# Kernel tuning notes

Measured on AMD Instinct MI355X. Metric: run time of the kernel, lower is better.

## Reference

```python
import jax, jax.numpy as jnp
import numpy as np

HEADS = 8
WS = 16
EPS = 1e-6


def setup_inputs() -> dict:
    key = jax.random.key(0)
    k1, k2 = jax.random.split(key)
    x = jax.random.normal(k1, (4, 64, 512, 512), dtype=jnp.float32)
    w_qkv = jax.random.normal(k2, (192, 64), dtype=jnp.float32) * 0.05  # 1x1 conv: [3*dim, dim]
    return {"x": x, "w_qkv": w_qkv}


def _elu1(t):
    return jax.nn.elu(t) + 1.0


def _lwmsa(x, w_qkv):
    B, C, H, W = x.shape
    ws, h = WS, HEADS
    d = C // h
    ph, pw = (-H) % ws, (-W) % ws
    if ph or pw:
        x = jnp.pad(x, ((0, 0), (0, 0), (0, ph), (0, pw)))
    Hp, Wp = H + ph, W + pw
    hh, ww = Hp // ws, Wp // ws
    # 1x1 conv == channel matmul
    qkv = jnp.einsum('oc,bchw->bohw', w_qkv, x)  # [B, 3C, Hp, Wp]
    # 'b (qkv h d) (hh ws1) (ww ws2) -> qkv (b hh ww) h d (ws1 ws2)'
    qkv = qkv.reshape(B, 3, h, d, hh, ws, ww, ws)
    qkv = qkv.transpose(1, 0, 4, 6, 2, 3, 5, 7).reshape(3, B * hh * ww, h, d, ws * ws)
    q, k, v = qkv[0], qkv[1], qkv[2]  # each [Bw, h, d, n]

    feat = None  # carried across heads, [Bw, d, n]
    feats = []
    for i in range(h):
        qi, ki, vi = q[:, i], k[:, i], v[:, i]
        if i > 0:
            qi, ki, vi = qi + feat, ki + feat, vi + feat
        qf = _elu1(qi).transpose(0, 2, 1)   # [Bw, n, d]
        kf = _elu1(ki)                      # [Bw, d, n]
        ksum = jnp.sum(kf, axis=-1) + EPS   # [Bw, d]
        # original: einsum('bhnm,bhc->bhn', q, ksum) sums m and c INDEPENDENTLY
        z = 1.0 / (jnp.sum(qf, axis=-1) * jnp.sum(ksum, axis=-1, keepdims=True))  # [Bw, n]
        kv = jnp.einsum('bdn,bcn->bdc', kf, vi)          # [Bw, d, d]
        feat = jnp.einsum('bnd,bdc,bn->bcn', qf, kv, z)  # [Bw, d, n]
        feats.append(feat)

    out = jnp.stack(feats, axis=1)  # [Bw, h, d, n]
    # '(b hh ww) h d (ws1 ws2) -> b (h d) (hh ws1) (ww ws2)'
    out = out.reshape(B, hh, ww, h, d, ws, ws)
    out = out.transpose(0, 3, 4, 1, 5, 2, 6).reshape(B, C, Hp, Wp)
    return out[:, :, :H, :W]


def reference(x, w_qkv):
    return _lwmsa(x, w_qkv)
```

## Files before the change

kernel.cpp:

```cpp
#include <hip/hip_runtime.h>

#define HW (512 * 512)
#define QP 260
#define WN 12288

typedef __bf16 bf16;
typedef __attribute__((ext_vector_type(8))) __bf16 bf16x8;
typedef __attribute__((ext_vector_type(4))) float f32x4;

__device__ __forceinline__ void cvt_split(float f, bf16& h, bf16& l) {
    h = (bf16)f;
    l = (bf16)(f - (float)h);
}

__global__ __launch_bounds__(256) void wcvt_kernel(
    const float* __restrict__ w, bf16* __restrict__ wh, bf16* __restrict__ wl)
{
    const int i = blockIdx.x * 256 + threadIdx.x;
    if (i < WN) {
        bf16 h, l;
        cvt_split(w[i], h, l);
        wh[i] = h;
        wl[i] = l;
    }
}

__global__ __launch_bounds__(256, 2) void lwmsa_kernel(
    const float* __restrict__ x,
    const bf16* __restrict__ wh,
    const bf16* __restrict__ wl,
    float* __restrict__ out)
{
    const int win  = blockIdx.x;
    const int b    = win >> 10;
    const int wrow = (win >> 5) & 31;
    const int wcol = win & 31;
    const int n    = threadIdx.x;
    const int lane = n & 63;
    const int wvid = n >> 6;
    const int c16  = lane & 15;
    const int q4   = lane >> 4;

    const int base = b * (64 * HW) + (wrow * 16 + (n >> 4)) * 512 + wcol * 16 + (n & 15);
    const int xwin = b * (64 * HW) + (wrow * 16) * 512 + wcol * 16;

    __shared__ float qk[24 * QP];
    __shared__ float kvp[4 * 64];
    __shared__ float kv_s[64];
    __shared__ float tp[2][4];

    bf16x8 ah[2][4], al[2][4];
    #pragma unroll
    for (int ks = 0; ks < 2; ++ks)
        #pragma unroll
        for (int mt = 0; mt < 4; ++mt) {
            const int row = wvid * 4 + mt;
            const float* xp = x + xwin + row * 512 + c16 + (ks * 32 + q4 * 8) * HW;
            #pragma unroll
            for (int j = 0; j < 8; ++j) {
                bf16 h, l;
                cvt_split(xp[j * HW], h, l);
                ah[ks][mt][j] = h;
                al[ks][mt][j] = l;
            }
        }

    auto mfma_stage = [&](int hh) {
        f32x4 acc[4][2];
        #pragma unroll
        for (int mt = 0; mt < 4; ++mt)
            #pragma unroll
            for (int nt = 0; nt < 2; ++nt)
                acc[mt][nt] = (f32x4){0.f, 0.f, 0.f, 0.f};

        #pragma unroll
        for (int ks = 0; ks < 2; ++ks) {
            #pragma unroll
            for (int nt = 0; nt < 2; ++nt) {
                const int ml   = nt * 16 + c16;
                const int grow = (ml < 24) ? ((ml >> 3) * 64 + hh * 8 + (ml & 7))
                                           : (hh * 8);
                const int off  = grow * 64 + ks * 32 + q4 * 8;
                const bf16x8 bh = *(const bf16x8*)&wh[off];
                const bf16x8 bl = *(const bf16x8*)&wl[off];
                #pragma unroll
                for (int mt = 0; mt < 4; ++mt) {
                    acc[mt][nt] = __builtin_amdgcn_mfma_f32_16x16x32_bf16(ah[ks][mt], bh, acc[mt][nt], 0, 0, 0);
                    acc[mt][nt] = __builtin_amdgcn_mfma_f32_16x16x32_bf16(al[ks][mt], bh, acc[mt][nt], 0, 0, 0);
                    acc[mt][nt] = __builtin_amdgcn_mfma_f32_16x16x32_bf16(ah[ks][mt], bl, acc[mt][nt], 0, 0, 0);
                }
            }
        }

        #pragma unroll
        for (int nt = 0; nt < 2; ++nt) {
            const int ml = nt * 16 + c16;
            if (ml < 24) {
                #pragma unroll
                for (int mt = 0; mt < 4; ++mt) {
                    const int px = (wvid * 4 + mt) * 16 + q4 * 4;
                    *(float4*)&qk[ml * QP + px] = *(float4*)&acc[mt][nt];
                }
            }
        }
    };

    float feat[8];
    #pragma unroll
    for (int d = 0; d < 8; ++d) feat[d] = 0.f;

    mfma_stage(0);
    __syncthreads();

    for (int h = 0; h < 8; ++h) {
        float qf[8];
        float Sq = 0.f, tpart = 0.f;
        #pragma unroll
        for (int d = 0; d < 8; ++d) {
            const float aq = qk[d * QP + n]        + feat[d];
            const float ak = qk[(8 + d) * QP + n]  + feat[d];
            const float av = qk[(16 + d) * QP + n] + feat[d];
            qf[d] = aq > 0.f ? aq + 1.f : __expf(aq);
            const float kf = ak > 0.f ? ak + 1.f : __expf(ak);
            Sq    += qf[d];
            tpart += kf;
            qk[(8 + d) * QP + n]  = kf;
            qk[(16 + d) * QP + n] = av;
        }

        #pragma unroll
        for (int off = 1; off < 64; off <<= 1)
            tpart += __shfl_xor(tpart, off, 64);
        if (lane == 0) tp[h & 1][wvid] = tpart;

        asm volatile("s_waitcnt lgkmcnt(0)" ::: "memory");

        {
            const float4* kr = (const float4*)(qk + (8 + (lane >> 3)) * QP + wvid * 64);
            const float4* vr = (const float4*)(qk + (16 + (lane & 7)) * QP + wvid * 64);
            float s0 = 0.f, s1 = 0.f, s2 = 0.f, s3 = 0.f;
            #pragma unroll
            for (int j = 0; j < 16; ++j) {
                const float4 kk = kr[j];
                const float4 vv = vr[j];
                s0 = fmaf(kk.x, vv.x, s0);
                s1 = fmaf(kk.y, vv.y, s1);
                s2 = fmaf(kk.z, vv.z, s2);
                s3 = fmaf(kk.w, vv.w, s3);
            }
            kvp[wvid * 64 + lane] = (s0 + s1) + (s2 + s3);
        }

        __syncthreads();

        if (n < 64)
            kv_s[n] = (kvp[n] + kvp[64 + n]) + (kvp[128 + n] + kvp[192 + n]);

        if (h < 7)
            mfma_stage(h + 1);

        __syncthreads();

        const float T  = ((tp[h & 1][0] + tp[h & 1][1]) + (tp[h & 1][2] + tp[h & 1][3])) + 8.0f * 1e-6f;
        const float zi = 1.0f / (Sq * T);

        float ft[8];
        #pragma unroll
        for (int d = 0; d < 8; ++d) ft[d] = 0.f;
        #pragma unroll
        for (int d = 0; d < 8; ++d) {
            const float qd = qf[d];
            const float4 a  = ((const float4*)(kv_s + d * 8))[0];
            const float4 bb = ((const float4*)(kv_s + d * 8))[1];
            ft[0] = fmaf(qd, a.x,  ft[0]);
            ft[1] = fmaf(qd, a.y,  ft[1]);
            ft[2] = fmaf(qd, a.z,  ft[2]);
            ft[3] = fmaf(qd, a.w,  ft[3]);
            ft[4] = fmaf(qd, bb.x, ft[4]);
            ft[5] = fmaf(qd, bb.y, ft[5]);
            ft[6] = fmaf(qd, bb.z, ft[6]);
            ft[7] = fmaf(qd, bb.w, ft[7]);
        }
        #pragma unroll
        for (int d = 0; d < 8; ++d) {
            feat[d] = ft[d] * zi;
            out[base + (h * 8 + d) * HW] = feat[d];
        }
    }
}

extern "C" void kernel_launch(void* const* d_in, const int* in_sizes, int n_in,
                              void* d_out, int out_size, void* d_ws, size_t ws_size,
                              hipStream_t stream) {
    const float* x  = (const float*)d_in[0];
    const float* w  = (const float*)d_in[1];
    float* out      = (float*)d_out;
    bf16* wh = (bf16*)d_ws;
    bf16* wl = wh + WN;
    wcvt_kernel<<<dim3((WN + 255) / 256), dim3(256), 0, stream>>>(w, wh, wl);
    lwmsa_kernel<<<dim3(4096), dim3(256), 0, stream>>>(x, wh, wl, out);
}
```

Before: 279.5 us.

## Process two adjacent windows per block to amortize syncs and weight loads

Each block now handles two horizontally adjacent 16x16 windows instead of one, so the grid shrinks from 4096 to 2048 blocks. Shared buffers, register fragments and per-head state are duplicated per window, and both windows' MFMA stages and reductions share the same barriers and weight-fragment loads. The aim is to amortize barrier latency and per-block overhead and to give each wave more independent work between syncs. In exchange it doubles register and LDS use (qk alone becomes about 50KB), which may cut occupancy below the two-blocks-per-CU launch bound.

```diff
diff --git a/kernel.cpp b/kernel.cpp
--- a/kernel.cpp
+++ b/kernel.cpp
@@ -31,41 +31,49 @@
     const bf16* __restrict__ wl,
     float* __restrict__ out)
 {
-    const int win  = blockIdx.x;
-    const int b    = win >> 10;
-    const int wrow = (win >> 5) & 31;
-    const int wcol = win & 31;
+    const int blk  = blockIdx.x;
+    const int b    = blk >> 9;
+    const int wrow = (blk >> 4) & 31;
+    const int wp   = blk & 15;
     const int n    = threadIdx.x;
     const int lane = n & 63;
     const int wvid = n >> 6;
     const int c16  = lane & 15;
     const int q4   = lane >> 4;
 
-    const int base = b * (64 * HW) + (wrow * 16 + (n >> 4)) * 512 + wcol * 16 + (n & 15);
-    const int xwin = b * (64 * HW) + (wrow * 16) * 512 + wcol * 16;
-
-    __shared__ float qk[24 * QP];
-    __shared__ float kvp[4 * 64];
-    __shared__ float kv_s[64];
-    __shared__ float tp[2][4];
-
-    bf16x8 ah[2][4], al[2][4];
+    __shared__ float qk[2][24 * QP];
+    __shared__ float kvp[2][4 * 64];
+    __shared__ float kv_s[2][64];
+    __shared__ float tp[2][2][4];
+
+    int base[2], xwin[2];
     #pragma unroll
-    for (int ks = 0; ks < 2; ++ks)
-        #pragma unroll
-        for (int mt = 0; mt < 4; ++mt) {
-            const int row = wvid * 4 + mt;
-            const float* xp = x + xwin + row * 512 + c16 + (ks * 32 + q4 * 8) * HW;
-            #pragma unroll
-            for (int j = 0; j < 8; ++j) {
-                bf16 h, l;
-                cvt_split(xp[j * HW], h, l);
-                ah[ks][mt][j] = h;
-                al[ks][mt][j] = l;
-            }
-        }
-
-    auto mfma_stage = [&](int hh) {
+    for (int w = 0; w < 2; ++w) {
+        const int wcol = wp * 2 + w;
+        base[w] = b * (64 * HW) + (wrow * 16 + (n >> 4)) * 512 + wcol * 16 + (n & 15);
+        xwin[w] = b * (64 * HW) + (wrow * 16) * 512 + wcol * 16;
+    }
+
+    bf16x8 ah[2][2][4], al[2][2][4];
+    #pragma unroll
+    for (int w = 0; w < 2; ++w)
+        #pragma unroll
+        for (int ks = 0; ks < 2; ++ks)
+            #pragma unroll
+            for (int mt = 0; mt < 4; ++mt) {
+                const int row = wvid * 4 + mt;
+                const float* xp = x + xwin[w] + row * 512 + c16 + (ks * 32 + q4 * 8) * HW;
+                #pragma unroll
+                for (int j = 0; j < 8; ++j) {
+                    bf16 h, l;
+                    cvt_split(xp[j * HW], h, l);
+                    ah[w][ks][mt][j] = h;
+                    al[w][ks][mt][j] = l;
+                }
+            }
+
+    auto mfma_stage = [&](const bf16x8 (&Ah)[2][4], const bf16x8 (&Al)[2][4],
+                          float* __restrict__ qkb, int hh) {
         f32x4 acc[4][2];
         #pragma unroll
         for (int mt = 0; mt < 4; ++mt)
@@ -85,9 +93,9 @@
                 const bf16x8 bl = *(const bf16x8*)&wl[off];
                 #pragma unroll
                 for (int mt = 0; mt < 4; ++mt) {
-                    acc[mt][nt] = __builtin_amdgcn_mfma_f32_16x16x32_bf16(ah[ks][mt], bh, acc[mt][nt], 0, 0, 0);
-                    acc[mt][nt] = __builtin_amdgcn_mfma_f32_16x16x32_bf16(al[ks][mt], bh, acc[mt][nt], 0, 0, 0);
-                    acc[mt][nt] = __builtin_amdgcn_mfma_f32_16x16x32_bf16(ah[ks][mt], bl, acc[mt][nt], 0, 0, 0);
+                    acc[mt][nt] = __builtin_amdgcn_mfma_f32_16x16x32_bf16(Ah[ks][mt], bh, acc[mt][nt], 0, 0, 0);
+                    acc[mt][nt] = __builtin_amdgcn_mfma_f32_16x16x32_bf16(Al[ks][mt], bh, acc[mt][nt], 0, 0, 0);
+                    acc[mt][nt] = __builtin_amdgcn_mfma_f32_16x16x32_bf16(Ah[ks][mt], bl, acc[mt][nt], 0, 0, 0);
                 }
             }
         }
@@ -99,45 +107,57 @@
                 #pragma unroll
                 for (int mt = 0; mt < 4; ++mt) {
                     const int px = (wvid * 4 + mt) * 16 + q4 * 4;
-                    *(float4*)&qk[ml * QP + px] = *(float4*)&acc[mt][nt];
+                    *(float4*)&qkb[ml * QP + px] = *(float4*)&acc[mt][nt];
                 }
             }
         }
     };
 
-    float feat[8];
+    float feat[2][8];
     #pragma unroll
-    for (int d = 0; d < 8; ++d) feat[d] = 0.f;
-
-    mfma_stage(0);
+    for (int w = 0; w < 2; ++w)
+        #pragma unroll
+        for (int d = 0; d < 8; ++d) feat[w][d] = 0.f;
+
+    mfma_stage(ah[0], al[0], qk[0], 0);
+    mfma_stage(ah[1], al[1], qk[1], 0);
     __syncthreads();
 
     for (int h = 0; h < 8; ++h) {
-        float qf[8];
-        float Sq = 0.f, tpart = 0.f;
-        #pragma unroll
-        for (int d = 0; d < 8; ++d) {
-            const float aq = qk[d * QP + n]        + feat[d];
-            const float ak = qk[(8 + d) * QP + n]  + feat[d];
-            const float av = qk[(16 + d) * QP + n] + feat[d];
-            qf[d] = aq > 0.f ? aq + 1.f : __expf(aq);
-            const float kf = ak > 0.f ? ak + 1.f : __expf(ak);
-            Sq    += qf[d];
-            tpart += kf;
-            qk[(8 + d) * QP + n]  = kf;
-            qk[(16 + d) * QP + n] = av;
-        }
-
-        #pragma unroll
-        for (int off = 1; off < 64; off <<= 1)
-            tpart += __shfl_xor(tpart, off, 64);
-        if (lane == 0) tp[h & 1][wvid] = tpart;
+        float qf[2][8], Sq[2], tpart[2];
+        #pragma unroll
+        for (int w = 0; w < 2; ++w) {
+            Sq[w] = 0.f; tpart[w] = 0.f;
+            #pragma unroll
+            for (int d = 0; d < 8; ++d) {
+                const float aq = qk[w][d * QP + n]        + feat[w][d];
+                const float ak = qk[w][(8 + d) * QP + n]  + feat[w][d];
+                const float av = qk[w][(16 + d) * QP + n] + feat[w][d];
+                qf[w][d] = aq > 0.f ? aq + 1.f : __expf(aq);
+                const float kf = ak > 0.f ? ak + 1.f : __expf(ak);
+                Sq[w]    += qf[w][d];
+                tpart[w] += kf;
+                qk[w][(8 + d) * QP + n]  = kf;
+                qk[w][(16 + d) * QP + n] = av;
+            }
+        }
+
+        #pragma unroll
+        for (int off = 1; off < 64; off <<= 1) {
+            tpart[0] += __shfl_xor(tpart[0], off, 64);
+            tpart[1] += __shfl_xor(tpart[1], off, 64);
+        }
+        if (lane == 0) {
+            tp[0][h & 1][wvid] = tpart[0];
+            tp[1][h & 1][wvid] = tpart[1];
+        }
 
         asm volatile("s_waitcnt lgkmcnt(0)" ::: "memory");
 
-        {
-            const float4* kr = (const float4*)(qk + (8 + (lane >> 3)) * QP + wvid * 64);
-            const float4* vr = (const float4*)(qk + (16 + (lane & 7)) * QP + wvid * 64);
+        #pragma unroll
+        for (int w = 0; w < 2; ++w) {
+            const float4* kr = (const float4*)(qk[w] + (8 + (lane >> 3)) * QP + wvid * 64);
+            const float4* vr = (const float4*)(qk[w] + (16 + (lane & 7)) * QP + wvid * 64);
             float s0 = 0.f, s1 = 0.f, s2 = 0.f, s3 = 0.f;
             #pragma unroll
             for (int j = 0; j < 16; ++j) {
@@ -148,43 +168,53 @@
                 s2 = fmaf(kk.z, vv.z, s2);
                 s3 = fmaf(kk.w, vv.w, s3);
             }
-            kvp[wvid * 64 + lane] = (s0 + s1) + (s2 + s3);
+            kvp[w][wvid * 64 + lane] = (s0 + s1) + (s2 + s3);
         }
 
         __syncthreads();
 
-        if (n < 64)
-            kv_s[n] = (kvp[n] + kvp[64 + n]) + (kvp[128 + n] + kvp[192 + n]);
-
-        if (h < 7)
-            mfma_stage(h + 1);
+        if (n < 64) {
+            kv_s[0][n] = (kvp[0][n] + kvp[0][64 + n]) + (kvp[0][128 + n] + kvp[0][192 + n]);
+        } else if (n < 128) {
+            const int m = n - 64;
+            kv_s[1][m] = (kvp[1][m] + kvp[1][64 + m]) + (kvp[1][128 + m] + kvp[1][192 + m]);
+        }
+
+        if (h < 7) {
+            mfma_stage(ah[0], al[0], qk[0], h + 1);
+            mfma_stage(ah[1], al[1], qk[1], h + 1);
+        }
 
         __syncthreads();
 
-        const float T  = ((tp[h & 1][0] + tp[h & 1][1]) + (tp[h & 1][2] + tp[h & 1][3])) + 8.0f * 1e-6f;
-        const float zi = 1.0f / (Sq * T);
-
-        float ft[8];
-        #pragma unroll
-        for (int d = 0; d < 8; ++d) ft[d] = 0.f;
-        #pragma unroll
-        for (int d = 0; d < 8; ++d) {
-            const float qd = qf[d];
-            const float4 a  = ((const float4*)(kv_s + d * 8))[0];
-            const float4 bb = ((const float4*)(kv_s + d * 8))[1];
-            ft[0] = fmaf(qd, a.x,  ft[0]);
-            ft[1] = fmaf(qd, a.y,  ft[1]);
-            ft[2] = fmaf(qd, a.z,  ft[2]);
-            ft[3] = fmaf(qd, a.w,  ft[3]);
-            ft[4] = fmaf(qd, bb.x, ft[4]);
-            ft[5] = fmaf(qd, bb.y, ft[5]);
-            ft[6] = fmaf(qd, bb.z, ft[6]);
-            ft[7] = fmaf(qd, bb.w, ft[7]);
-        }
-        #pragma unroll
-        for (int d = 0; d < 8; ++d) {
-            feat[d] = ft[d] * zi;
-            out[base + (h * 8 + d) * HW] = feat[d];
+        #pragma unroll
+        for (int w = 0; w < 2; ++w) {
+            const float T  = ((tp[w][h & 1][0] + tp[w][h & 1][1]) +
+                              (tp[w][h & 1][2] + tp[w][h & 1][3])) + 8.0f * 1e-6f;
+            const float zi = 1.0f / (Sq[w] * T);
+
+            float ft[8];
+            #pragma unroll
+            for (int d = 0; d < 8; ++d) ft[d] = 0.f;
+            #pragma unroll
+            for (int d = 0; d < 8; ++d) {
+                const float qd = qf[w][d];
+                const float4 a  = ((const float4*)(kv_s[w] + d * 8))[0];
+                const float4 bb = ((const float4*)(kv_s[w] + d * 8))[1];
+                ft[0] = fmaf(qd, a.x,  ft[0]);
+                ft[1] = fmaf(qd, a.y,  ft[1]);
+                ft[2] = fmaf(qd, a.z,  ft[2]);
+                ft[3] = fmaf(qd, a.w,  ft[3]);
+                ft[4] = fmaf(qd, bb.x, ft[4]);
+                ft[5] = fmaf(qd, bb.y, ft[5]);
+                ft[6] = fmaf(qd, bb.z, ft[6]);
+                ft[7] = fmaf(qd, bb.w, ft[7]);
+            }
+            #pragma unroll
+            for (int d = 0; d < 8; ++d) {
+                feat[w][d] = ft[d] * zi;
+                out[base[w] + (h * 8 + d) * HW] = feat[w][d];
+            }
         }
     }
 }
@@ -198,5 +228,5 @@
     bf16* wh = (bf16*)d_ws;
     bf16* wl = wh + WN;
     wcvt_kernel<<<dim3((WN + 255) / 256), dim3(256), 0, stream>>>(w, wh, wl);
-    lwmsa_kernel<<<dim3(4096), dim3(256), 0, stream>>>(x, wh, wl, out);
-}
+    lwmsa_kernel<<<dim3(2048), dim3(256), 0, stream>>>(x, wh, wl, out);
+}
```

Result: faster. 256.6 us (-8.2%).

## Double-buffer qkv shared tiles to drop one barrier per head

Applied to the files above, without the earlier changes.

Shared q/k/v staging and the kv partial sums become double-buffered by head parity, so the next head's MFMA projection can write into the other buffer before the barrier. Each wavefront then reduces the four kv partials into its own private copy of kv_s, which removes the second __syncthreads per head. This trades extra LDS (roughly doubling the qk footprint, which may lower occupancy) and redundant per-wave reductions for fewer block-wide barriers.

```diff
diff --git a/kernel.cpp b/kernel.cpp
--- a/kernel.cpp
+++ b/kernel.cpp
@@ -44,9 +44,9 @@
     const int base = b * (64 * HW) + (wrow * 16 + (n >> 4)) * 512 + wcol * 16 + (n & 15);
     const int xwin = b * (64 * HW) + (wrow * 16) * 512 + wcol * 16;
 
-    __shared__ float qk[24 * QP];
-    __shared__ float kvp[4 * 64];
-    __shared__ float kv_s[64];
+    __shared__ float qk[2][24 * QP];
+    __shared__ float kvp[2][256];
+    __shared__ float kv_s[256];
     __shared__ float tp[2][4];
 
     bf16x8 ah[2][4], al[2][4];
@@ -65,7 +65,7 @@
             }
         }
 
-    auto mfma_stage = [&](int hh) {
+    auto mfma_stage = [&](int hh, int par) {
         f32x4 acc[4][2];
         #pragma unroll
         for (int mt = 0; mt < 4; ++mt)
@@ -99,7 +99,7 @@
                 #pragma unroll
                 for (int mt = 0; mt < 4; ++mt) {
                     const int px = (wvid * 4 + mt) * 16 + q4 * 4;
-                    *(float4*)&qk[ml * QP + px] = *(float4*)&acc[mt][nt];
+                    *(float4*)&qk[par][ml * QP + px] = *(float4*)&acc[mt][nt];
                 }
             }
         }
@@ -109,35 +109,37 @@
     #pragma unroll
     for (int d = 0; d < 8; ++d) feat[d] = 0.f;
 
-    mfma_stage(0);
+    mfma_stage(0, 0);
     __syncthreads();
 
     for (int h = 0; h < 8; ++h) {
+        const int p = h & 1;
+
         float qf[8];
         float Sq = 0.f, tpart = 0.f;
         #pragma unroll
         for (int d = 0; d < 8; ++d) {
-            const float aq = qk[d * QP + n]        + feat[d];
-            const float ak = qk[(8 + d) * QP + n]  + feat[d];
-            const float av = qk[(16 + d) * QP + n] + feat[d];
+            const float aq = qk[p][d * QP + n]        + feat[d];
+            const float ak = qk[p][(8 + d) * QP + n]  + feat[d];
+            const float av = qk[p][(16 + d) * QP + n] + feat[d];
             qf[d] = aq > 0.f ? aq + 1.f : __expf(aq);
             const float kf = ak > 0.f ? ak + 1.f : __expf(ak);
             Sq    += qf[d];
             tpart += kf;
-            qk[(8 + d) * QP + n]  = kf;
-            qk[(16 + d) * QP + n] = av;
+            qk[p][(8 + d) * QP + n]  = kf;
+            qk[p][(16 + d) * QP + n] = av;
         }
 
         #pragma unroll
         for (int off = 1; off < 64; off <<= 1)
             tpart += __shfl_xor(tpart, off, 64);
-        if (lane == 0) tp[h & 1][wvid] = tpart;
+        if (lane == 0) tp[p][wvid] = tpart;
 
         asm volatile("s_waitcnt lgkmcnt(0)" ::: "memory");
 
         {
-            const float4* kr = (const float4*)(qk + (8 + (lane >> 3)) * QP + wvid * 64);
-            const float4* vr = (const float4*)(qk + (16 + (lane & 7)) * QP + wvid * 64);
+            const float4* kr = (const float4*)(qk[p] + (8 + (lane >> 3)) * QP + wvid * 64);
+            const float4* vr = (const float4*)(qk[p] + (16 + (lane & 7)) * QP + wvid * 64);
             float s0 = 0.f, s1 = 0.f, s2 = 0.f, s3 = 0.f;
             #pragma unroll
             for (int j = 0; j < 16; ++j) {
@@ -148,20 +150,22 @@
                 s2 = fmaf(kk.z, vv.z, s2);
                 s3 = fmaf(kk.w, vv.w, s3);
             }
-            kvp[wvid * 64 + lane] = (s0 + s1) + (s2 + s3);
-        }
+            kvp[p][wvid * 64 + lane] = (s0 + s1) + (s2 + s3);
+        }
+
+        if (h < 7)
+            mfma_stage(h + 1, p ^ 1);
 
         __syncthreads();
 
-        if (n < 64)
-            kv_s[n] = (kvp[n] + kvp[64 + n]) + (kvp[128 + n] + kvp[192 + n]);
-
-        if (h < 7)
-            mfma_stage(h + 1);
-
-        __syncthreads();
-
-        const float T  = ((tp[h & 1][0] + tp[h & 1][1]) + (tp[h & 1][2] + tp[h & 1][3])) + 8.0f * 1e-6f;
+        {
+            const float kvsum = (kvp[p][lane] + kvp[p][64 + lane]) +
+                                (kvp[p][128 + lane] + kvp[p][192 + lane]);
+            kv_s[wvid * 64 + lane] = kvsum;
+        }
+        asm volatile("s_waitcnt lgkmcnt(0)" ::: "memory");
+
+        const float T  = ((tp[p][0] + tp[p][1]) + (tp[p][2] + tp[p][3])) + 8.0f * 1e-6f;
         const float zi = 1.0f / (Sq * T);
 
         float ft[8];
@@ -170,8 +174,8 @@
         #pragma unroll
         for (int d = 0; d < 8; ++d) {
             const float qd = qf[d];
-            const float4 a  = ((const float4*)(kv_s + d * 8))[0];
-            const float4 bb = ((const float4*)(kv_s + d * 8))[1];
+            const float4 a  = ((const float4*)(kv_s + wvid * 64 + d * 8))[0];
+            const float4 bb = ((const float4*)(kv_s + wvid * 64 + d * 8))[1];
             ft[0] = fmaf(qd, a.x,  ft[0]);
             ft[1] = fmaf(qd, a.y,  ft[1]);
             ft[2] = fmaf(qd, a.z,  ft[2]);
```

Result: slower. 299.6 us (+7.2%).
